# Kernel optimization log

Measured on AMD Instinct MI355X. Metric: run time of the kernel, lower is better.

## Reference

```python
import jax, jax.numpy as jnp
import numpy as np

MAX_SHIFT = 4.0  # init max_shift; stored shifts are pre-divided by it
Q = 3            # Maclaurin order


def setup_inputs() -> dict:
    key = jax.random.key(0)
    k1, k2, k3, k4 = jax.random.split(key, 4)
    x = jax.random.normal(k1, (16, 64, 112, 112), jnp.float32)
    # weights: (out_channels, q*in_channels, k, k)
    weights = jax.random.normal(k2, (128, 192, 3, 3), jnp.float32) * 0.05
    bias = jax.random.normal(k3, (128,), jnp.float32) * 0.05
    # stored shifts buffer: uniform(-max_shift, max_shift) then /= max_shift -> [-1, 1]
    shifts = jax.random.uniform(k4, (64, 2), jnp.float32, -1.0, 1.0)
    return {"x": x, "weights": weights, "bias": bias, "shifts": shifts}


def _shift_one_channel(xc, sx, sy):
    """Bilinear translate one channel by (sx, sy) pixels, zero padding.
    Equivalent to F.affine_grid(identity + [sx/(W/2), sy/(H/2)]) + grid_sample
    (align_corners=False): out[n, i, j] = x[n, i + sy, j + sx] (bilinear).
    xc: (N, H, W)."""
    N, H, W = xc.shape
    jx = jnp.arange(W, dtype=xc.dtype) + sx  # sampled x coord per output col
    iy = jnp.arange(H, dtype=xc.dtype) + sy  # sampled y coord per output row
    x0f = jnp.floor(jx)
    y0f = jnp.floor(iy)
    wx = jx - x0f  # (W,)
    wy = iy - y0f  # (H,)
    x0 = x0f.astype(jnp.int32)
    y0 = y0f.astype(jnp.int32)

    def gather(yi, xi):
        vy = (yi >= 0) & (yi < H)
        vx = (xi >= 0) & (xi < W)
        yc = jnp.clip(yi, 0, H - 1)
        xcl = jnp.clip(xi, 0, W - 1)
        v = xc[:, yc, :][:, :, xcl]  # (N, H, W)
        return v * (vy[:, None] & vx[None, :]).astype(xc.dtype)

    return ((1 - wy)[:, None] * (1 - wx)[None, :] * gather(y0, x0)
            + (1 - wy)[:, None] * wx[None, :] * gather(y0, x0 + 1)
            + wy[:, None] * (1 - wx)[None, :] * gather(y0 + 1, x0)
            + wy[:, None] * wx[None, :] * gather(y0 + 1, x0 + 1))


def reference(x, weights, bias, shifts):
    s = shifts * MAX_SHIFT  # pixel shifts, (C_in, 2) = (sx, sy)
    # per-channel bilinear shift (vmap over channel axis)
    shifted = jax.vmap(_shift_one_channel, in_axes=(1, 0, 0), out_axes=1)(
        x, s[:, 0], s[:, 1])  # (N, C, H, W)
    # Maclaurin powers concatenated along channels: (N, q*C, H, W)
    y = jnp.concatenate([shifted ** i for i in range(1, Q + 1)], axis=1)
    out = jax.lax.conv_general_dilated(
        y, weights, window_strides=(1, 1), padding=[(1, 1), (1, 1)],
        dimension_numbers=("NCHW", "OIHW", "NCHW"))
    return out + bias[None, :, None, None]
```

## Files before the change

kernel.cpp:

```cpp
#include <hip/hip_runtime.h>
#include <hip/hip_bf16.h>

typedef __bf16 bf16x8 __attribute__((ext_vector_type(8)));
typedef float  f32x4  __attribute__((ext_vector_type(4)));

#define H_DIM 112
#define W_DIM 112
#define CIN 64
#define CMID 192
#define COUT 128
#define NB 16

__device__ __forceinline__ void dma16(const void* g, void* l) {
    __builtin_amdgcn_global_load_lds(
        (const __attribute__((address_space(1))) unsigned*)g,
        (__attribute__((address_space(3))) unsigned*)l, 16, 0, 0);
}

__global__ __launch_bounds__(256) void repack_w_kernel(
    const float* __restrict__ w, __hip_bfloat16* __restrict__ wr)
{
    int idx = blockIdx.x * 256 + threadIdx.x;
    if (idx < 9 * COUT * CMID) {
        int ci  = idx % CMID;
        int t   = idx / CMID;
        int co  = t % COUT;
        int khw = t / COUT;
        wr[idx] = __float2bfloat16(w[(co * CMID + ci) * 9 + khw]);
    }
}

__global__ __launch_bounds__(256) void shift_pow_kernel(
    const float* __restrict__ x, const float* __restrict__ shifts,
    __hip_bfloat16* __restrict__ y)
{
    __shared__ __align__(16) __hip_bfloat16 tile[112 * 104];

    const int tid = threadIdx.x;
    const int h   = blockIdx.x;
    const int cb  = blockIdx.y * 32;
    const int n   = blockIdx.z;

    const int c  = tid >> 3;
    const int l8 = tid & 7;

    const float sx = shifts[2 * (cb + c)]     * 4.0f;
    const float sy = shifts[2 * (cb + c) + 1] * 4.0f;
    const float fx = floorf(sx), fy = floorf(sy);
    const int   ix = (int)fx,    iy = (int)fy;
    const float wx = sx - fx,    wy = sy - fy;

    const int r0 = h + iy, r1 = r0 + 1;
    const float vy0 = ((unsigned)r0 < (unsigned)H_DIM) ? 1.f : 0.f;
    const float vy1 = ((unsigned)r1 < (unsigned)H_DIM) ? 1.f : 0.f;
    const float ww00 = (1.f - wy) * (1.f - wx) * vy0;
    const float ww01 = (1.f - wy) * wx         * vy0;
    const float ww10 = wy         * (1.f - wx) * vy1;
    const float ww11 = wy         * wx         * vy1;

    const float* bx   = x + (size_t)(n * CIN + cb + c) * (H_DIM * W_DIM);
    const float* row0 = bx + min(max(r0, 0), H_DIM - 1) * W_DIM;
    const float* row1 = bx + min(max(r1, 0), H_DIM - 1) * W_DIM;

    #pragma unroll
    for (int k = 0; k < 14; ++k) {
        int px = l8 + 8 * k;
        int q0 = px + ix, q1 = q0 + 1;
        float f0 = ((unsigned)q0 < (unsigned)W_DIM) ? 1.f : 0.f;
        float f1 = ((unsigned)q1 < (unsigned)W_DIM) ? 1.f : 0.f;
        int a0 = min(max(q0, 0), W_DIM - 1);
        int a1 = min(max(q1, 0), W_DIM - 1);
        float v = f0 * (ww00 * row0[a0] + ww10 * row1[a0])
                + f1 * (ww01 * row0[a1] + ww11 * row1[a1]);
        float v2 = v * v, v3 = v2 * v;
        __hip_bfloat16* tp = &tile[px * 104];
        tp[c]      = __float2bfloat16(v);
        tp[c + 32] = __float2bfloat16(v2);
        tp[c + 64] = __float2bfloat16(v3);
    }
    __syncthreads();

    const float4* tl4 = (const float4*)tile;
    float4* yo4 = (float4*)(y + ((size_t)(n * H_DIM + h) * W_DIM) * CMID);
    const int cbd4 = cb >> 3;
    #pragma unroll
    for (int k = 0; k < 6; ++k) {
        int i = k * 256 + tid;
        if (i < 1344) {
            int px  = i / 12;
            int cp4 = i - px * 12;
            int chunk = cp4 >> 2, e4 = cp4 & 3;
            yo4[px * 24 + chunk * 8 + cbd4 + e4] = tl4[px * 13 + cp4];
        }
    }
}

#define YSTR_E 104
#define BUF_E  12288

#define CONV_GROUP(G, CUR, NXT) do {                                          \
    const int c3_ = (G) / 3, kw_ = (G) % 3;                                   \
    if ((G) < 8) {                                                            \
        const int c3n_ = ((G) + 1) / 3, kwn_ = ((G) + 1) % 3;                 \
        _Pragma("unroll")                                                     \
        for (int nt = 0; nt < 7; ++nt)                                        \
            NXT[nt] = *(const bf16x8*)(lbase +                                \
                (nt * 16 + kwn_) * YSTR_E + c3n_ * 32);                       \
    }                                                                         \
    _Pragma("unroll")                                                         \
    for (int nt = 0; nt < 7; ++nt) {                                          \
        acc[0][nt] = __builtin_amdgcn_mfma_f32_16x16x32_bf16(                 \
            af[c3_][kw_][0], CUR[nt], acc[0][nt], 0, 0, 0);                   \
        acc[1][nt] = __builtin_amdgcn_mfma_f32_16x16x32_bf16(                 \
            af[c3_][kw_][1], CUR[nt], acc[1][nt], 0, 0, 0);                   \
    }                                                                         \
    if ((G) < 8) {                                                            \
        _Pragma("unroll")                                                     \
        for (int k_ = 0; k_ < 7; ++k_) {                                      \
            __builtin_amdgcn_sched_group_barrier(0x100, 1, 0);   \
            __builtin_amdgcn_sched_group_barrier(0x008, 2, 0);    \
        }                                                                     \
    } else {                                                                  \
        __builtin_amdgcn_sched_group_barrier(0x008, 14, 0);                   \
    }                                                                         \
} while (0)

__global__ __launch_bounds__(256, 2) void conv_kernel(
    const __bf16* __restrict__ y,
    const __bf16* __restrict__ wr,
    const float* __restrict__ bias,
    float* __restrict__ out)
{
    __shared__ __align__(16) __bf16 ybuf[2][BUF_E];

    const int tid  = threadIdx.x;
    const int lane = tid & 63;
    const int wid  = tid >> 6;
    const int m    = lane & 15;
    const int quad = lane >> 4;

    const int bid = blockIdx.x;
    const int id  = (bid & 7) * 224 + (bid >> 3);
    const int n   = id / H_DIM;
    const int h   = id - n * H_DIM;

    if (tid < 208) {
        int b    = tid >= 104;
        int r    = tid - b * 104;
        int slot = (r >= 52) ? 113 : 0;
        int dw   = (r >= 52) ? r - 52 : r;
        ((unsigned*)&ybuf[b][0])[slot * 52 + dw] = 0u;
    }

    int dj[6];
    #pragma unroll
    for (int j = 0; j < 6; ++j) {
        int t = 4 * j + wid;
        int o = 208 + 1024 * t + 16 * lane;
        int slot = o / 208;
        int rem  = o - slot * 208;
        dj[j] = (t < 23 && rem < 192 && slot <= 112)
                    ? ((slot - 1) * 384 + rem) : -1;
    }

    f32x4 acc[2][7];
    #pragma unroll
    for (int mt = 0; mt < 2; ++mt)
        #pragma unroll
        for (int nt = 0; nt < 7; ++nt)
            #pragma unroll
            for (int r = 0; r < 4; ++r) acc[mt][nt][r] = 0.0f;

    const char* ybase = (const char*)y + (size_t)n * (H_DIM * W_DIM * CMID * 2);

    const int f = (h == 0)         ? 2 : 0;
    const int l = (h == H_DIM - 1) ? 3 : 5;

    {
        int row = h + (f >> 1) - 1, half = f & 1;
        const char* src = ybase + (size_t)row * (W_DIM * CMID * 2) + half * 192;
        char* lb = (char*)&ybuf[0][0];
        #pragma unroll
        for (int j = 0; j < 6; ++j) {
            int t = 4 * j + wid;
            if (dj[j] >= 0) dma16(src + dj[j], lb + 208 + 1024 * t);
        }
    }
    __syncthreads();

    int buf = 0;
    for (int s = f; s <= l; ++s) {
        const int kh = s >> 1, half = s & 1;

        bf16x8 af[3][3][2];
        #pragma unroll
        for (int c3 = 0; c3 < 3; ++c3)
            #pragma unroll
            for (int kw = 0; kw < 3; ++kw)
                #pragma unroll
                for (int mt = 0; mt < 2; ++mt)
                    af[c3][kw][mt] = *(const bf16x8*)(
                        wr + (size_t)((kh * 3 + kw) * COUT + wid * 32 + mt * 16 + m) * CMID
                           + half * 96 + c3 * 32 + quad * 8);

        __builtin_amdgcn_sched_barrier(0);

        if (s < l) {
            int row = h + ((s + 1) >> 1) - 1, halfn = (s + 1) & 1;
            const char* src = ybase + (size_t)row * (W_DIM * CMID * 2) + halfn * 192;
            char* lb = (char*)&ybuf[buf ^ 1][0];
            #pragma unroll
            for (int j = 0; j < 6; ++j) {
                int t = 4 * j + wid;
                if (dj[j] >= 0) dma16(src + dj[j], lb + 208 + 1024 * t);
            }
        }

        const __bf16* lbase = &ybuf[buf][m * YSTR_E + quad * 8];

        bf16x8 bA[7], bB[7];
        #pragma unroll
        for (int nt = 0; nt < 7; ++nt)
            bA[nt] = *(const bf16x8*)(lbase + (nt * 16 + 0) * YSTR_E + 0 * 32);
        __builtin_amdgcn_sched_group_barrier(0x100, 7, 0);

        CONV_GROUP(0, bA, bB);
        CONV_GROUP(1, bB, bA);
        CONV_GROUP(2, bA, bB);
        CONV_GROUP(3, bB, bA);
        CONV_GROUP(4, bA, bB);
        CONV_GROUP(5, bB, bA);
        CONV_GROUP(6, bA, bB);
        CONV_GROUP(7, bB, bA);
        CONV_GROUP(8, bA, bB);

        __syncthreads();
        buf ^= 1;
    }

    #pragma unroll
    for (int mt = 0; mt < 2; ++mt) {
        const int co0 = wid * 32 + mt * 16 + quad * 4;
        float bv[4];
        #pragma unroll
        for (int rr = 0; rr < 4; ++rr) bv[rr] = bias[co0 + rr];
        #pragma unroll
        for (int nt = 0; nt < 7; ++nt) {
            int j = nt * 16 + m;
            #pragma unroll
            for (int rr = 0; rr < 4; ++rr) {
                out[(((size_t)n * COUT + co0 + rr) * H_DIM + h) * W_DIM + j] =
                    acc[mt][nt][rr] + bv[rr];
            }
        }
    }
}

extern "C" void kernel_launch(void* const* d_in, const int* in_sizes, int n_in,
                              void* d_out, int out_size, void* d_ws, size_t ws_size,
                              hipStream_t stream) {
    const float* x      = (const float*)d_in[0];
    const float* w      = (const float*)d_in[1];
    const float* bias   = (const float*)d_in[2];
    const float* shifts = (const float*)d_in[3];
    float* out = (float*)d_out;

    __hip_bfloat16* y  = (__hip_bfloat16*)d_ws;
    __hip_bfloat16* wr = (__hip_bfloat16*)((char*)d_ws + 77070336);

    repack_w_kernel<<<dim3((9 * COUT * CMID + 255) / 256), 256, 0, stream>>>(w, wr);
    shift_pow_kernel<<<dim3(H_DIM, 2, NB), 256, 0, stream>>>(x, shifts, y);
    conv_kernel<<<dim3(H_DIM * NB), 256, 0, stream>>>(
        (const __bf16*)y, (const __bf16*)wr, bias, out);
}
```

Measured before the change: 296.4 us.

## Fuse bilinear shift and power expansion into conv kernel, drop intermediate tensor

Removes the separate shift_pow kernel and its large bf16 intermediate in global memory. The conv kernel now computes each shifted row half (powers 1-3) directly into the LDS double buffer from x, replacing the async global-to-LDS DMA. This cuts the write and re-read of the intermediate tensor. In exchange each row's shift is recomputed up to three times across neighbouring output rows, and the compute now runs synchronously with scalar LDS stores instead of asynchronous DMA.

```diff
diff --git a/kernel.cpp b/kernel.cpp
--- a/kernel.cpp
+++ b/kernel.cpp
@@ -10,12 +10,6 @@
 #define CMID 192
 #define COUT 128
 #define NB 16
-
-__device__ __forceinline__ void dma16(const void* g, void* l) {
-    __builtin_amdgcn_global_load_lds(
-        (const __attribute__((address_space(1))) unsigned*)g,
-        (__attribute__((address_space(3))) unsigned*)l, 16, 0, 0);
-}
 
 __global__ __launch_bounds__(256) void repack_w_kernel(
     const float* __restrict__ w, __hip_bfloat16* __restrict__ wr)
@@ -30,73 +24,58 @@
     }
 }
 
-__global__ __launch_bounds__(256) void shift_pow_kernel(
-    const float* __restrict__ x, const float* __restrict__ shifts,
-    __hip_bfloat16* __restrict__ y)
+#define YSTR_E 104
+#define YLDS_E (114 * 104)
+
+__device__ __forceinline__ void compute_half(
+    int row, int half, __bf16* dstb, const float* bx,
+    int ix, int iy, float wx, float wy, int cc, int pg)
 {
-    __shared__ __align__(16) __hip_bfloat16 tile[112 * 104];
-
-    const int tid = threadIdx.x;
-    const int h   = blockIdx.x;
-    const int cb  = blockIdx.y * 32;
-    const int n   = blockIdx.z;
-
-    const int c  = tid >> 3;
-    const int l8 = tid & 7;
-
-    const float sx = shifts[2 * (cb + c)]     * 4.0f;
-    const float sy = shifts[2 * (cb + c) + 1] * 4.0f;
-    const float fx = floorf(sx), fy = floorf(sy);
-    const int   ix = (int)fx,    iy = (int)fy;
-    const float wx = sx - fx,    wy = sy - fy;
-
-    const int r0 = h + iy, r1 = r0 + 1;
-    const float vy0 = ((unsigned)r0 < (unsigned)H_DIM) ? 1.f : 0.f;
-    const float vy1 = ((unsigned)r1 < (unsigned)H_DIM) ? 1.f : 0.f;
-    const float ww00 = (1.f - wy) * (1.f - wx) * vy0;
-    const float ww01 = (1.f - wy) * wx         * vy0;
-    const float ww10 = wy         * (1.f - wx) * vy1;
-    const float ww11 = wy         * wx         * vy1;
-
-    const float* bx   = x + (size_t)(n * CIN + cb + c) * (H_DIM * W_DIM);
+    int r0 = row + iy, r1 = r0 + 1;
+    float vy0 = ((unsigned)r0 < (unsigned)H_DIM) ? 1.f : 0.f;
+    float vy1 = ((unsigned)r1 < (unsigned)H_DIM) ? 1.f : 0.f;
+    float omwx = 1.f - wx, omwy = 1.f - wy;
+    float ww00 = omwy * omwx * vy0;
+    float ww01 = omwy * wx   * vy0;
+    float ww10 = wy * omwx * vy1;
+    float ww11 = wy * wx   * vy1;
     const float* row0 = bx + min(max(r0, 0), H_DIM - 1) * W_DIM;
     const float* row1 = bx + min(max(r1, 0), H_DIM - 1) * W_DIM;
-
-    #pragma unroll
-    for (int k = 0; k < 14; ++k) {
-        int px = l8 + 8 * k;
-        int q0 = px + ix, q1 = q0 + 1;
-        float f0 = ((unsigned)q0 < (unsigned)W_DIM) ? 1.f : 0.f;
-        float f1 = ((unsigned)q1 < (unsigned)W_DIM) ? 1.f : 0.f;
-        int a0 = min(max(q0, 0), W_DIM - 1);
-        int a1 = min(max(q1, 0), W_DIM - 1);
-        float v = f0 * (ww00 * row0[a0] + ww10 * row1[a0])
-                + f1 * (ww01 * row0[a1] + ww11 * row1[a1]);
-        float v2 = v * v, v3 = v2 * v;
-        __hip_bfloat16* tp = &tile[px * 104];
-        tp[c]      = __float2bfloat16(v);
-        tp[c + 32] = __float2bfloat16(v2);
-        tp[c + 64] = __float2bfloat16(v3);
-    }
-    __syncthreads();
-
-    const float4* tl4 = (const float4*)tile;
-    float4* yo4 = (float4*)(y + ((size_t)(n * H_DIM + h) * W_DIM) * CMID);
-    const int cbd4 = cb >> 3;
-    #pragma unroll
-    for (int k = 0; k < 6; ++k) {
-        int i = k * 256 + tid;
-        if (i < 1344) {
-            int px  = i / 12;
-            int cp4 = i - px * 12;
-            int chunk = cp4 >> 2, e4 = cp4 & 3;
-            yo4[px * 24 + chunk * 8 + cbd4 + e4] = tl4[px * 13 + cp4];
-        }
-    }
-}
-
-#define YSTR_E 104
-#define BUF_E  12288
+    __hip_bfloat16* dst = (__hip_bfloat16*)dstb;
+
+    if (half == 0) {
+        #pragma unroll 7
+        for (int p = 0; p < 28; ++p) {
+            int px = pg * 28 + p;
+            int q0 = px + ix, q1 = q0 + 1;
+            float f0 = ((unsigned)q0 < (unsigned)W_DIM) ? 1.f : 0.f;
+            float f1 = ((unsigned)q1 < (unsigned)W_DIM) ? 1.f : 0.f;
+            int a0 = min(max(q0, 0), W_DIM - 1);
+            int a1 = min(max(q1, 0), W_DIM - 1);
+            float v = f0 * (ww00 * row0[a0] + ww10 * row1[a0])
+                    + f1 * (ww01 * row0[a1] + ww11 * row1[a1]);
+            __hip_bfloat16* bp = dst + (px + 1) * YSTR_E;
+            bp[cc] = __float2bfloat16(v);
+            if (cc < 32) bp[64 + cc] = __float2bfloat16(v * v);
+        }
+    } else {
+        #pragma unroll 7
+        for (int p = 0; p < 28; ++p) {
+            int px = pg * 28 + p;
+            int q0 = px + ix, q1 = q0 + 1;
+            float f0 = ((unsigned)q0 < (unsigned)W_DIM) ? 1.f : 0.f;
+            float f1 = ((unsigned)q1 < (unsigned)W_DIM) ? 1.f : 0.f;
+            int a0 = min(max(q0, 0), W_DIM - 1);
+            int a1 = min(max(q1, 0), W_DIM - 1);
+            float v = f0 * (ww00 * row0[a0] + ww10 * row1[a0])
+                    + f1 * (ww01 * row0[a1] + ww11 * row1[a1]);
+            float v2 = v * v;
+            __hip_bfloat16* bp = dst + (px + 1) * YSTR_E;
+            if (cc >= 32) bp[cc - 32] = __float2bfloat16(v2);
+            bp[32 + cc] = __float2bfloat16(v2 * v);
+        }
+    }
+}
 
 #define CONV_GROUP(G, CUR, NXT) do {                                          \
     const int c3_ = (G) / 3, kw_ = (G) % 3;                                   \
@@ -126,12 +105,13 @@
 } while (0)
 
 __global__ __launch_bounds__(256, 2) void conv_kernel(
-    const __bf16* __restrict__ y,
+    const float* __restrict__ x,
     const __bf16* __restrict__ wr,
     const float* __restrict__ bias,
+    const float* __restrict__ shifts,
     float* __restrict__ out)
 {
-    __shared__ __align__(16) __bf16 ybuf[2][BUF_E];
+    __shared__ __align__(16) __bf16 ybuf[2][YLDS_E];
 
     const int tid  = threadIdx.x;
     const int lane = tid & 63;
@@ -143,6 +123,15 @@
     const int id  = (bid & 7) * 224 + (bid >> 3);
     const int n   = id / H_DIM;
     const int h   = id - n * H_DIM;
+
+    const int cc = tid & 63;
+    const int pg = tid >> 6;
+    const float sx = shifts[2 * cc]     * 4.0f;
+    const float sy = shifts[2 * cc + 1] * 4.0f;
+    const float fxf = floorf(sx), fyf = floorf(sy);
+    const int   ix = (int)fxf,    iy = (int)fyf;
+    const float wxp = sx - fxf,   wyp = sy - fyf;
+    const float* bx = x + (size_t)(n * CIN + cc) * (H_DIM * W_DIM);
 
     if (tid < 208) {
         int b    = tid >= 104;
@@ -152,17 +141,6 @@
         ((unsigned*)&ybuf[b][0])[slot * 52 + dw] = 0u;
     }
 
-    int dj[6];
-    #pragma unroll
-    for (int j = 0; j < 6; ++j) {
-        int t = 4 * j + wid;
-        int o = 208 + 1024 * t + 16 * lane;
-        int slot = o / 208;
-        int rem  = o - slot * 208;
-        dj[j] = (t < 23 && rem < 192 && slot <= 112)
-                    ? ((slot - 1) * 384 + rem) : -1;
-    }
-
     f32x4 acc[2][7];
     #pragma unroll
     for (int mt = 0; mt < 2; ++mt)
@@ -171,27 +149,21 @@
             #pragma unroll
             for (int r = 0; r < 4; ++r) acc[mt][nt][r] = 0.0f;
 
-    const char* ybase = (const char*)y + (size_t)n * (H_DIM * W_DIM * CMID * 2);
-
     const int f = (h == 0)         ? 2 : 0;
     const int l = (h == H_DIM - 1) ? 3 : 5;
 
-    {
-        int row = h + (f >> 1) - 1, half = f & 1;
-        const char* src = ybase + (size_t)row * (W_DIM * CMID * 2) + half * 192;
-        char* lb = (char*)&ybuf[0][0];
-        #pragma unroll
-        for (int j = 0; j < 6; ++j) {
-            int t = 4 * j + wid;
-            if (dj[j] >= 0) dma16(src + dj[j], lb + 208 + 1024 * t);
-        }
-    }
+    compute_half(h + (f >> 1) - 1, f & 1, &ybuf[0][0],
+                 bx, ix, iy, wxp, wyp, cc, pg);
     __syncthreads();
 
     int buf = 0;
     for (int s = f; s <= l; ++s) {
+        if (s < l) {
+            compute_half(h + ((s + 1) >> 1) - 1, (s + 1) & 1,
+                         &ybuf[buf ^ 1][0], bx, ix, iy, wxp, wyp, cc, pg);
+        }
+
         const int kh = s >> 1, half = s & 1;
-
         bf16x8 af[3][3][2];
         #pragma unroll
         for (int c3 = 0; c3 < 3; ++c3)
@@ -202,19 +174,6 @@
                     af[c3][kw][mt] = *(const bf16x8*)(
                         wr + (size_t)((kh * 3 + kw) * COUT + wid * 32 + mt * 16 + m) * CMID
                            + half * 96 + c3 * 32 + quad * 8);
-
-        __builtin_amdgcn_sched_barrier(0);
-
-        if (s < l) {
-            int row = h + ((s + 1) >> 1) - 1, halfn = (s + 1) & 1;
-            const char* src = ybase + (size_t)row * (W_DIM * CMID * 2) + halfn * 192;
-            char* lb = (char*)&ybuf[buf ^ 1][0];
-            #pragma unroll
-            for (int j = 0; j < 6; ++j) {
-                int t = 4 * j + wid;
-                if (dj[j] >= 0) dma16(src + dj[j], lb + 208 + 1024 * t);
-            }
-        }
 
         const __bf16* lbase = &ybuf[buf][m * YSTR_E + quad * 8];
 
@@ -265,11 +224,9 @@
     const float* shifts = (const float*)d_in[3];
     float* out = (float*)d_out;
 
-    __hip_bfloat16* y  = (__hip_bfloat16*)d_ws;
-    __hip_bfloat16* wr = (__hip_bfloat16*)((char*)d_ws + 77070336);
+    __hip_bfloat16* wr = (__hip_bfloat16*)d_ws;
 
     repack_w_kernel<<<dim3((9 * COUT * CMID + 255) / 256), 256, 0, stream>>>(w, wr);
-    shift_pow_kernel<<<dim3(H_DIM, 2, NB), 256, 0, stream>>>(x, shifts, y);
     conv_kernel<<<dim3(H_DIM * NB), 256, 0, stream>>>(
-        (const __bf16*)y, (const __bf16*)wr, bias, out);
-}
+        x, (const __bf16*)wr, bias, shifts, out);
+}
```

Measured after the change: 777.6 us. 2.62x slower.
